# Performance work log

Hardware: AMD Instinct MI355X
Metric: run time of the kernel (lower is better)

The kernel has to match this reference:

```python
import jax, jax.numpy as jnp
import numpy as np

BLOCK = 256


def setup_inputs() -> dict:
    key = jax.random.key(0)
    ks = jax.random.split(key, 6)
    b, n, hid = 2, 4096, 2048
    h, d = 16, 128
    x = jax.random.normal(ks[0], (b, n, hid), dtype=jnp.float32)
    slope_rate = jax.random.uniform(ks[1], (h, 1, 1), dtype=jnp.float32)
    Wqkv = jax.random.normal(ks[2], (3 * h * d, hid), dtype=jnp.float32) * 0.02
    Wg = jax.random.normal(ks[3], (h * d, hid), dtype=jnp.float32) * 0.02
    norm_w = jnp.ones((h * d,), dtype=jnp.float32)
    Wo = jax.random.normal(ks[4], (hid, h * d), dtype=jnp.float32) * 0.02
    return {"x": x, "slope_rate": slope_rate, "Wqkv": Wqkv, "Wg": Wg, "norm_w": norm_w, "Wo": Wo}


def reference(x, slope_rate, Wqkv, Wg, norm_w, Wo):
    b, n, hid = x.shape
    h = slope_rate.shape[0]
    d = Wqkv.shape[0] // (3 * h)
    nb = n // BLOCK

    qkv = jax.nn.silu(x @ Wqkv.T).reshape(b, n, h, 3 * d)
    q, k, v = jnp.split(qkv, 3, axis=-1)           # each (b, n, h, d)
    # -> (b, h, n, d)
    q = q.transpose(0, 2, 1, 3)
    k = k.transpose(0, 2, 1, 3)
    v = v.transpose(0, 2, 1, 3)

    s = slope_rate.astype(jnp.float32)             # (h, 1, 1)
    arr = jnp.arange(1, BLOCK + 1, dtype=jnp.float32)
    q_decay = jnp.exp(-s * arr[:, None])           # (h, BLOCK, 1)
    k_decay = jnp.exp(-s * (BLOCK - arr[:, None])) # (h, BLOCK, 1)
    idx = arr[:, None] - arr[None, :]              # (BLOCK, BLOCK)
    diag_decay = jnp.where(idx >= 0, jnp.exp(-s * idx), 0.0)  # (h, BLOCK, BLOCK)
    block_decay = jnp.exp(-s * BLOCK)              # (h, 1, 1)

    # chunk into blocks: (nb, b, h, BLOCK, d)
    def chunk(t):
        return t.reshape(b, h, nb, BLOCK, d).transpose(2, 0, 1, 3, 4)
    qc, kc, vc = chunk(q), chunk(k), chunk(v)

    def step(kv, qkv_blk):
        qi, ki, vi = qkv_blk
        # inter-block: decayed query against running kv state
        out_nd = jnp.einsum('bhmd,bhde->bhme', qi * q_decay, kv)
        # intra-block: decay-masked quadratic attention
        qk = jnp.einsum('bhmd,bhnd->bhmn', qi, ki) * diag_decay
        out_d = jnp.einsum('bhmn,bhne->bhme', qk, vi)
        kv_new = block_decay * kv + jnp.einsum('bhmd,bhme->bhde', ki * k_decay, vi)
        return kv_new, out_nd + out_d

    kv0 = jnp.zeros((b, h, d, d), dtype=jnp.float32)
    _, out_blocks = jax.lax.scan(step, kv0, (qc, kc, vc))  # (nb, b, h, BLOCK, d)

    out = out_blocks.transpose(1, 2, 0, 3, 4).reshape(b, h, n, d)
    out = out.transpose(0, 2, 1, 3).reshape(b, n, h * d)  # b n (h d)

    # RMSNorm
    eps = jnp.finfo(jnp.float32).eps
    rms = jax.lax.rsqrt(jnp.mean(out * out, axis=-1, keepdims=True) + eps)
    out = out * rms * norm_w

    gate = jax.nn.sigmoid(x @ Wg.T)
    return (gate * out) @ Wo.T
```

## Files before the change

kernel.cpp:

```cpp
#include <hip/hip_runtime.h>
#include <stdint.h>

typedef __attribute__((ext_vector_type(8))) short short8;
typedef __attribute__((ext_vector_type(4))) float f32x4;

#define DEV static __device__ __forceinline__

DEV float b2f(unsigned short u) {
  unsigned x = ((unsigned)u) << 16;
  return __builtin_bit_cast(float, x);
}
DEV unsigned short f2b(float f) {
  unsigned x = __builtin_bit_cast(unsigned, f);
  return (unsigned short)((x + 0x7fffu + ((x >> 16) & 1u)) >> 16);
}
DEV void gload16(const unsigned short* g, unsigned short* l) {
  __builtin_amdgcn_global_load_lds((const __attribute__((address_space(1))) void*)g,
                                   (__attribute__((address_space(3))) void*)l, 16, 0, 0);
}
#define MFMA(a, b, c) __builtin_amdgcn_mfma_f32_16x16x32_bf16(a, b, c, 0, 0, 0)
#define BARRIER                          \
  asm volatile("" ::: "memory");         \
  __builtin_amdgcn_s_barrier();          \
  asm volatile("" ::: "memory")

__global__ __launch_bounds__(256) void k_f2b4(const float* __restrict__ x,
                                              const float* __restrict__ wqkv,
                                              const float* __restrict__ wg,
                                              const float* __restrict__ wo,
                                              unsigned short* __restrict__ dst) {
  long gi = ((long)blockIdx.x * 256 + threadIdx.x) * 4;
  const float* src;
  long off;
  if (gi < 16777216L) { src = x; off = gi; }
  else if (gi < 29360128L) { src = wqkv; off = gi - 16777216L; }
  else if (gi < 33554432L) { src = wg; off = gi - 29360128L; }
  else { src = wo; off = gi - 33554432L; }
  float4 f = *(const float4*)(src + off);
  ushort4 o;
  o.x = f2b(f.x); o.y = f2b(f.y); o.z = f2b(f.z); o.w = f2b(f.w);
  *(ushort4*)(dst + gi) = o;
}

template <int MODE>
__global__ __launch_bounds__(512, 2) void k_gemm(
    const unsigned short* __restrict__ A, const unsigned short* __restrict__ B0,
    const unsigned short* __restrict__ B1,
    unsigned short* __restrict__ o_q, unsigned short* __restrict__ o_k,
    unsigned short* __restrict__ o_v, unsigned short* __restrict__ o_g,
    float* __restrict__ o_f) {
  const int K = 2048, NT = 64;
  __shared__ unsigned short sm[65536];
  int tid = threadIdx.x, w = tid >> 6, lane = tid & 63;
  int wm = w >> 2, wn = w & 3;
  int l15 = lane & 15, l4 = lane >> 4;
  int xcd = blockIdx.x & 7, sub = blockIdx.x >> 3;
  int tm = xcd * 4 + (sub & 3), tn = sub >> 2;
  int brow = tm << 8, bcol = tn << 8;
  const unsigned short* Ab = A + (size_t)brow * K;
  const unsigned short* Bb = (MODE == 1 || bcol < 6144) ? (B0 + (size_t)bcol * K)
                                                        : (B1 + (size_t)(bcol - 6144) * K);
  f32x4 acc[8][4];
#pragma unroll
  for (int m = 0; m < 8; m++)
#pragma unroll
    for (int n = 0; n < 4; n++) acc[m][n] = (f32x4)0.f;

  int rdA[4], rdB[4];
  const int bslotb = (wn >> 1) ? 24576 : 8192;
  const int bposb = (wn & 1) * 64;
#pragma unroll
  for (int fi = 0; fi < 4; ++fi) {
    int posA = wm * 64 + fi * 16 + l15;
    rdA[fi] = posA * 64 + ((l4 ^ ((posA >> 1) & 3)) << 4);
    int posB = bposb + fi * 16 + l15;
    rdB[fi] = bslotb + posB * 64 + ((l4 ^ ((posB >> 1) & 3)) << 4);
  }
  const unsigned short* gP[4];
  {
    int pos = tid >> 2, pb = tid & 3;
    int scol = (pb ^ ((pos >> 1) & 3)) << 3;
#pragma unroll
    for (int s = 0; s < 4; ++s) {
      const unsigned short* gb = (s & 1) ? Bb : Ab;
      int ro = (s >> 1) << 7;
      gP[s] = gb + (size_t)(ro + pos) * K + scol;
    }
  }
  const int dLb = tid * 16;

  auto stage = [&](int bufbyte) {
#pragma unroll
    for (int s = 0; s < 4; ++s) {
      gload16(gP[s], (unsigned short*)((char*)sm + bufbyte + s * 8192 + dLb));
      gP[s] += 32;
    }
  };

  stage(0);
  stage(32768);
  asm volatile("s_waitcnt vmcnt(4)" ::: "memory");
  BARRIER;

  int b0 = 0, b1 = 32768, b2 = 65536;
  for (int T = 0; T < NT; ++T) {
    stage(b2);
    const char* smb = (const char*)sm + b0;
    short8 bfr[4], afA[4], afB[4];
#pragma unroll
    for (int nj = 0; nj < 4; ++nj) bfr[nj] = *(const short8*)(smb + rdB[nj]);
#pragma unroll
    for (int fi = 0; fi < 4; ++fi) afA[fi] = *(const short8*)(smb + rdA[fi]);
#pragma unroll
    for (int fi = 0; fi < 4; ++fi) afB[fi] = *(const short8*)(smb + (rdA[fi] + 16384));
    __builtin_amdgcn_s_setprio(1);
#pragma unroll
    for (int mi = 0; mi < 4; ++mi)
#pragma unroll
      for (int nj = 0; nj < 4; ++nj) acc[mi][nj] = MFMA(afA[mi], bfr[nj], acc[mi][nj]);
#pragma unroll
    for (int mi = 0; mi < 4; ++mi)
#pragma unroll
      for (int nj = 0; nj < 4; ++nj) acc[4 + mi][nj] = MFMA(afB[mi], bfr[nj], acc[4 + mi][nj]);
    __builtin_amdgcn_s_setprio(0);
    asm volatile("s_waitcnt vmcnt(4)" ::: "memory");
    BARRIER;
    int t = b0; b0 = b1; b1 = b2; b2 = t;
  }
  asm volatile("s_waitcnt vmcnt(0)" ::: "memory");
  BARRIER;

  if (MODE == 0) {
#pragma unroll
    for (int mf = 0; mf < 8; ++mf) {
      int rowb = (mf >> 2) * 128 + wm * 64 + (mf & 3) * 16 + l4 * 4;
#pragma unroll
      for (int ni = 0; ni < 4; ++ni) {
        int cx = wn * 64 + ((ni ^ l4) << 4) + l15;
        int colg = bcol + wn * 64 + ni * 16 + l15;
#pragma unroll
        for (int r = 0; r < 4; ++r) {
          float v = acc[mf][ni][r];
          float a = (colg < 6144) ? v / (1.f + __expf(-v))
                                  : 1.f / (1.f + __expf(-v));
          sm[(rowb + r) * 256 + cx] = f2b(a);
        }
      }
    }
    BARRIER;
    int rl0 = tid >> 5;
    int ch = (tid & 31) * 8;
    int cg = bcol + ch;
    unsigned short* qkvb = nullptr;
    size_t hbase = 0;
    int off = 0;
    const bool isq = (cg < 6144);
    if (isq) {
      int hh = cg / 384, dd = cg - hh * 384;
      int sel = dd >> 7;
      off = dd & 127;
      qkvb = (sel == 0) ? o_q : (sel == 1) ? o_k : o_v;
      hbase = (size_t)hh * 4096;
    }
#pragma unroll
    for (int it = 0; it < 16; ++it) {
      int rl = it * 16 + rl0;
      int cx = ch ^ (((rl >> 2) & 3) << 4);
      short8 v8 = *(const short8*)(sm + rl * 256 + cx);
      int row = brow + rl;
      if (isq) {
        int b = row >> 12, t = row & 4095;
        *(short8*)(qkvb + ((size_t)b * 65536 + hbase + t) * 128 + off) = v8;
      } else {
        *(short8*)(o_g + (size_t)row * 2048 + (cg - 6144)) = v8;
      }
    }
  } else {
#pragma unroll
    for (int mf = 0; mf < 8; ++mf)
#pragma unroll
      for (int r = 0; r < 4; ++r) {
        int row = brow + (mf >> 2) * 128 + wm * 64 + (mf & 3) * 16 + l4 * 4 + r;
#pragma unroll
        for (int ni = 0; ni < 4; ++ni) {
          int col = bcol + wn * 64 + ni * 16 + l15;
          o_f[(size_t)row * 2048 + col] = acc[mf][ni][r];
        }
      }
  }
}

__global__ __launch_bounds__(256) void k_kvblk(const unsigned short* __restrict__ kk,
                                               const unsigned short* __restrict__ vv,
                                               const float* __restrict__ slope,
                                               unsigned short* __restrict__ kvT) {
  int gid = blockIdx.x;
  int bh = gid >> 4, blk = gid & 15;
  float s = slope[bh & 15];
  __shared__ unsigned short kT[128][72];
  __shared__ unsigned short vT[128][72];
  int tid = threadIdx.x, w = tid >> 6, lane = tid & 63;
  int wrow = (w >> 1) * 64, wcol = (w & 1) * 64;
  f32x4 acc[4][4];
#pragma unroll
  for (int m = 0; m < 4; m++)
#pragma unroll
    for (int n = 0; n < 4; n++) acc[m][n] = (f32x4)0.f;
  const unsigned short* kb = kk + ((size_t)bh * 4096 + blk * 256) * 128;
  const unsigned short* vb = vv + ((size_t)bh * 4096 + blk * 256) * 128;
  int tt = tid & 63, c0 = (tid >> 6) * 32;
  for (int tc = 0; tc < 4; ++tc) {
    __syncthreads();
    int tg = tc * 64 + tt;
    float kd = __expf(-s * (float)(255 - tg));
#pragma unroll
    for (int g = 0; g < 4; ++g) {
      int c = c0 + g * 8;
      short8 k8 = *(const short8*)(kb + (size_t)tg * 128 + c);
      short8 v8 = *(const short8*)(vb + (size_t)tg * 128 + c);
#pragma unroll
      for (int j = 0; j < 8; ++j) {
        kT[c + j][tt] = f2b(b2f((unsigned short)k8[j]) * kd);
        vT[c + j][tt] = (unsigned short)v8[j];
      }
    }
    __syncthreads();
#pragma unroll
    for (int kx = 0; kx < 64; kx += 32) {
      int ko = kx + (lane >> 4) * 8;
      short8 af[4], bfr[4];
#pragma unroll
      for (int m = 0; m < 4; m++) af[m] = *(const short8*)&vT[wrow + m * 16 + (lane & 15)][ko];
#pragma unroll
      for (int n = 0; n < 4; n++) bfr[n] = *(const short8*)&kT[wcol + n * 16 + (lane & 15)][ko];
#pragma unroll
      for (int m = 0; m < 4; m++)
#pragma unroll
        for (int n = 0; n < 4; n++) acc[m][n] = MFMA(af[m], bfr[n], acc[m][n]);
    }
  }
  unsigned short* op = kvT + (size_t)gid * 16384;
#pragma unroll
  for (int m = 0; m < 4; m++)
#pragma unroll
    for (int r = 0; r < 4; r++) {
      int e = wrow + m * 16 + (lane >> 4) * 4 + r;
#pragma unroll
      for (int n = 0; n < 4; n++) {
        int d = wcol + n * 16 + (lane & 15);
        op[e * 128 + d] = f2b(acc[m][n][r]);
      }
    }
}

__global__ void k_scan(unsigned short* kvT, const float* __restrict__ slope) {
  int gid = blockIdx.x;
  int bh = gid >> 6;
  int eo = (gid & 63) * 256 + threadIdx.x;
  float s = slope[bh & 15];
  float bd = __expf(-s * 256.f);
  float st = 0.f;
  size_t base = (size_t)bh * 16 * 16384 + eo;
#pragma unroll
  for (int i = 0; i < 16; ++i) {
    unsigned short c = kvT[base + (size_t)i * 16384];
    kvT[base + (size_t)i * 16384] = f2b(st);
    st = bd * st + b2f(c);
  }
}

__global__ __launch_bounds__(256) void k_attn(const unsigned short* __restrict__ q,
                                              const unsigned short* __restrict__ kk,
                                              const unsigned short* __restrict__ vv,
                                              const unsigned short* __restrict__ kvT,
                                              const float* __restrict__ slope,
                                              unsigned short* __restrict__ attn) {
  int gid = blockIdx.x;
  int hf = gid & 1, blk = (gid >> 1) & 15, bh = gid >> 5;
  float s = slope[bh & 15];
  __shared__ unsigned short k_sh[64][136];
  __shared__ unsigned short vT_sh[128][72];
  __shared__ unsigned short s_sh[4][32][72];
  int tid = threadIdx.x, w = tid >> 6, lane = tid & 63;
  int mm0 = hf * 128 + w * 32;
  const unsigned short* qb = q + ((size_t)bh * 4096 + blk * 256) * 128;
  const unsigned short* kvb = kvT + (size_t)(bh * 16 + blk) * 16384;
  f32x4 acc[2][8];
#pragma unroll
  for (int m = 0; m < 2; m++)
#pragma unroll
    for (int n = 0; n < 8; n++) acc[m][n] = (f32x4)0.f;
#pragma unroll
  for (int kx = 0; kx < 128; kx += 32) {
    int ko = kx + (lane >> 4) * 8;
    short8 af[2], bfr[8];
#pragma unroll
    for (int mi = 0; mi < 2; mi++)
      af[mi] = *(const short8*)(qb + (size_t)(mm0 + mi * 16 + (lane & 15)) * 128 + ko);
#pragma unroll
    for (int ni = 0; ni < 8; ni++)
      bfr[ni] = *(const short8*)(kvb + (size_t)(ni * 16 + (lane & 15)) * 128 + ko);
#pragma unroll
    for (int mi = 0; mi < 2; mi++)
#pragma unroll
      for (int ni = 0; ni < 8; ni++) acc[mi][ni] = MFMA(af[mi], bfr[ni], acc[mi][ni]);
  }
#pragma unroll
  for (int mi = 0; mi < 2; mi++)
#pragma unroll
    for (int r = 0; r < 4; r++) {
      float qd = __expf(-s * (float)(mm0 + mi * 16 + (lane >> 4) * 4 + r + 1));
#pragma unroll
      for (int ni = 0; ni < 8; ni++) acc[mi][ni][r] *= qd;
    }
  int nchunk = 2 * (hf + 1);
  for (int tc = 0; tc < nchunk; ++tc) {
    __syncthreads();
    {
      int t2 = tid >> 2, c = (tid & 3) * 32;
      const unsigned short* kp = kk + ((size_t)bh * 4096 + blk * 256 + tc * 64 + t2) * 128 + c;
#pragma unroll
      for (int g = 0; g < 4; ++g) *(short8*)&k_sh[t2][c + g * 8] = *(const short8*)(kp + g * 8);
    }
    {
      int t2 = tid & 63, e0 = (tid >> 6) * 32;
      const unsigned short* vp = vv + ((size_t)bh * 4096 + blk * 256 + tc * 64 + t2) * 128 + e0;
#pragma unroll
      for (int g = 0; g < 4; ++g) {
        short8 v8 = *(const short8*)(vp + g * 8);
#pragma unroll
        for (int j = 0; j < 8; ++j) vT_sh[e0 + g * 8 + j][t2] = (unsigned short)v8[j];
      }
    }
    __syncthreads();
    if (tc * 64 <= mm0 + 31) {
      f32x4 sa[2][4];
#pragma unroll
      for (int m = 0; m < 2; m++)
#pragma unroll
        for (int n = 0; n < 4; n++) sa[m][n] = (f32x4)0.f;
#pragma unroll
      for (int kx = 0; kx < 128; kx += 32) {
        int ko = kx + (lane >> 4) * 8;
        short8 af[2], bfr[4];
#pragma unroll
        for (int mi = 0; mi < 2; mi++)
          af[mi] = *(const short8*)(qb + (size_t)(mm0 + mi * 16 + (lane & 15)) * 128 + ko);
#pragma unroll
        for (int ni = 0; ni < 4; ni++) bfr[ni] = *(const short8*)&k_sh[ni * 16 + (lane & 15)][ko];
#pragma unroll
        for (int mi = 0; mi < 2; mi++)
#pragma unroll
          for (int ni = 0; ni < 4; ni++) sa[mi][ni] = MFMA(af[mi], bfr[ni], sa[mi][ni]);
      }
#pragma unroll
      for (int mi = 0; mi < 2; mi++)
#pragma unroll
        for (int ni = 0; ni < 4; ni++)
#pragma unroll
          for (int r = 0; r < 4; r++) {
            int mm = mm0 + mi * 16 + (lane >> 4) * 4 + r;
            int ttg = tc * 64 + ni * 16 + (lane & 15);
            int diff = mm - ttg;
            float val = (diff >= 0) ? sa[mi][ni][r] * __expf(-s * (float)diff) : 0.f;
            s_sh[w][mi * 16 + (lane >> 4) * 4 + r][ni * 16 + (lane & 15)] = f2b(val);
          }
#pragma unroll
      for (int k2 = 0; k2 < 64; k2 += 32) {
        int ko2 = k2 + (lane >> 4) * 8;
        short8 a2[2];
#pragma unroll
        for (int mi = 0; mi < 2; mi++)
          a2[mi] = *(const short8*)&s_sh[w][mi * 16 + (lane & 15)][ko2];
#pragma unroll
        for (int ni = 0; ni < 8; ni++) {
          short8 b2 = *(const short8*)&vT_sh[ni * 16 + (lane & 15)][ko2];
#pragma unroll
          for (int mi = 0; mi < 2; mi++) acc[mi][ni] = MFMA(a2[mi], b2, acc[mi][ni]);
        }
      }
    }
  }
  int b = bh >> 4, h = bh & 15;
#pragma unroll
  for (int mi = 0; mi < 2; mi++)
#pragma unroll
    for (int r = 0; r < 4; r++) {
      int mm = mm0 + mi * 16 + (lane >> 4) * 4 + r;
      size_t rowp = ((size_t)b * 4096 + blk * 256 + mm) * 2048 + h * 128;
#pragma unroll
      for (int ni = 0; ni < 8; ni++) attn[rowp + ni * 16 + (lane & 15)] = f2b(acc[mi][ni][r]);
    }
}

__global__ __launch_bounds__(256) void k_norm(const unsigned short* __restrict__ attn,
                                              const unsigned short* __restrict__ gate,
                                              const float* __restrict__ nw,
                                              unsigned short* __restrict__ y) {
  int row = blockIdx.x;
  int tid = threadIdx.x, w = tid >> 6, lane = tid & 63;
  const unsigned short* ap = attn + (size_t)row * 2048 + tid * 8;
  const unsigned short* gp = gate + (size_t)row * 2048 + tid * 8;
  short8 a8 = *(const short8*)ap;
  float vals[8];
  float ss = 0.f;
#pragma unroll
  for (int j = 0; j < 8; ++j) {
    vals[j] = b2f((unsigned short)a8[j]);
    ss += vals[j] * vals[j];
  }
#pragma unroll
  for (int off = 32; off > 0; off >>= 1) ss += __shfl_down(ss, off, 64);
  __shared__ float red[4];
  if (lane == 0) red[w] = ss;
  __syncthreads();
  float tot = red[0] + red[1] + red[2] + red[3];
  float rms = rsqrtf(tot * (1.f / 2048.f) + 1.1920929e-07f);
  short8 g8 = *(const short8*)gp;
  short8 o;
#pragma unroll
  for (int j = 0; j < 8; ++j)
    o[j] = (short)f2b(vals[j] * rms * nw[tid * 8 + j] * b2f((unsigned short)g8[j]));
  *(short8*)(y + (size_t)row * 2048 + tid * 8) = o;
}

extern "C" void kernel_launch(void* const* d_in, const int* in_sizes, int n_in, void* d_out,
                              int out_size, void* d_ws, size_t ws_size, hipStream_t stream) {
  const float* x = (const float*)d_in[0];
  const float* slope = (const float*)d_in[1];
  const float* Wqkv = (const float*)d_in[2];
  const float* Wg = (const float*)d_in[3];
  const float* nw = (const float*)d_in[4];
  const float* Wo = (const float*)d_in[5];
  float* out = (float*)d_out;

  unsigned short* q = (unsigned short*)d_ws;
  unsigned short* k = q + 16777216;
  unsigned short* v = k + 16777216;
  unsigned short* gate = v + 16777216;
  unsigned short* xb = gate + 16777216;
  unsigned short* wqkvb = xb + 16777216;
  unsigned short* wgb = wqkvb + 12582912;
  unsigned short* wob = wgb + 4194304;
  unsigned short* kvT = wob + 4194304;
  unsigned short* attn = wqkvb;
  unsigned short* y = xb;

  k_f2b4<<<36864, 256, 0, stream>>>(x, Wqkv, Wg, Wo, xb);

  k_gemm<0><<<1024, 512, 0, stream>>>(xb, wqkvb, wgb, q, k, v, gate, nullptr);
  k_kvblk<<<512, 256, 0, stream>>>(k, v, slope, kvT);
  k_scan<<<2048, 256, 0, stream>>>(kvT, slope);
  k_attn<<<1024, 256, 0, stream>>>(q, k, v, kvT, slope, attn);
  k_norm<<<8192, 256, 0, stream>>>(attn, gate, nw, y);
  k_gemm<1><<<256, 512, 0, stream>>>(y, wob, nullptr, nullptr, nullptr, nullptr, nullptr, out);
}
```

Measured before the change: 469.9 us.

## Register-double-buffer GEMM LDS fragments; merge attention halves into 512-thread blocks

The main GEMM loop moves to a four-buffer LDS ring with three stages in flight. It is unrolled by two and ping-pongs two register fragment sets, so the LDS reads for the next tile overlap the MFMAs of the current one. The attention kernel now uses one 512-thread block per 256-row chunk instead of two 256-thread halves, so K/V tiles are loaded into LDS once and shared. Its output is staged through swizzled LDS so global stores are 16-byte coalesced rows. The cost is more LDS per block and more registers, which can lower occupancy, plus extra barriers in the attention epilogue.

After: 467.4 us. Within noise of the previous version (-0.5%).

```diff
diff --git a/kernel.cpp b/kernel.cpp
--- a/kernel.cpp
+++ b/kernel.cpp
@@ -97,38 +97,49 @@
     }
   };
 
-  stage(0);
-  stage(32768);
+  short8 cA0[4], cA1[4], cB[4], nA0[4], nA1[4], nB[4];
+#define LDTILE(dA0, dA1, dB, bufbyte)                                              \
+  {                                                                                \
+    const char* _b = (const char*)sm + (bufbyte);                                  \
+    _Pragma("unroll") for (int fi = 0; fi < 4; ++fi) {                             \
+      dB[fi] = *(const short8*)(_b + rdB[fi]);                                     \
+      dA0[fi] = *(const short8*)(_b + rdA[fi]);                                    \
+      dA1[fi] = *(const short8*)(_b + (rdA[fi] + 16384));                          \
+    }                                                                              \
+  }
+#define MFMATILE(sA0, sA1, sB)                                                     \
+  {                                                                                \
+    __builtin_amdgcn_s_setprio(1);                                                 \
+    _Pragma("unroll") for (int mi = 0; mi < 4; ++mi)                               \
+        _Pragma("unroll") for (int nj = 0; nj < 4; ++nj)                           \
+            acc[mi][nj] = MFMA(sA0[mi], sB[nj], acc[mi][nj]);                      \
+    _Pragma("unroll") for (int mi = 0; mi < 4; ++mi)                               \
+        _Pragma("unroll") for (int nj = 0; nj < 4; ++nj)                           \
+            acc[4 + mi][nj] = MFMA(sA1[mi], sB[nj], acc[4 + mi][nj]);              \
+    __builtin_amdgcn_s_setprio(0);                                                 \
+  }
+
+  stage(0); stage(32768); stage(65536);
   asm volatile("s_waitcnt vmcnt(4)" ::: "memory");
   BARRIER;
-
-  int b0 = 0, b1 = 32768, b2 = 65536;
-  for (int T = 0; T < NT; ++T) {
-    stage(b2);
-    const char* smb = (const char*)sm + b0;
-    short8 bfr[4], afA[4], afB[4];
-#pragma unroll
-    for (int nj = 0; nj < 4; ++nj) bfr[nj] = *(const short8*)(smb + rdB[nj]);
-#pragma unroll
-    for (int fi = 0; fi < 4; ++fi) afA[fi] = *(const short8*)(smb + rdA[fi]);
-#pragma unroll
-    for (int fi = 0; fi < 4; ++fi) afB[fi] = *(const short8*)(smb + (rdA[fi] + 16384));
-    __builtin_amdgcn_s_setprio(1);
-#pragma unroll
-    for (int mi = 0; mi < 4; ++mi)
-#pragma unroll
-      for (int nj = 0; nj < 4; ++nj) acc[mi][nj] = MFMA(afA[mi], bfr[nj], acc[mi][nj]);
-#pragma unroll
-    for (int mi = 0; mi < 4; ++mi)
-#pragma unroll
-      for (int nj = 0; nj < 4; ++nj) acc[4 + mi][nj] = MFMA(afB[mi], bfr[nj], acc[4 + mi][nj]);
-    __builtin_amdgcn_s_setprio(0);
+  LDTILE(cA0, cA1, cB, 0);
+
+  for (int T = 0; T < NT; T += 2) {
+    stage(((T + 3) & 3) * 32768);
+    LDTILE(nA0, nA1, nB, ((T + 1) & 3) * 32768);
+    MFMATILE(cA0, cA1, cB);
     asm volatile("s_waitcnt vmcnt(4)" ::: "memory");
     BARRIER;
-    int t = b0; b0 = b1; b1 = b2; b2 = t;
+    stage(((T + 4) & 3) * 32768);
+    LDTILE(cA0, cA1, cB, ((T + 2) & 3) * 32768);
+    MFMATILE(nA0, nA1, nB);
+    asm volatile("s_waitcnt vmcnt(4)" ::: "memory");
+    BARRIER;
   }
   asm volatile("s_waitcnt vmcnt(0)" ::: "memory");
   BARRIER;
+#undef LDTILE
+#undef MFMATILE
 
   if (MODE == 0) {
 #pragma unroll
@@ -269,20 +280,22 @@
   }
 }
 
-__global__ __launch_bounds__(256) void k_attn(const unsigned short* __restrict__ q,
+__global__ __launch_bounds__(512) void k_attn(const unsigned short* __restrict__ q,
                                               const unsigned short* __restrict__ kk,
                                               const unsigned short* __restrict__ vv,
                                               const unsigned short* __restrict__ kvT,
                                               const float* __restrict__ slope,
                                               unsigned short* __restrict__ attn) {
   int gid = blockIdx.x;
-  int hf = gid & 1, blk = (gid >> 1) & 15, bh = gid >> 5;
+  int blk = gid & 15, bh = gid >> 4;
   float s = slope[bh & 15];
-  __shared__ unsigned short k_sh[64][136];
-  __shared__ unsigned short vT_sh[128][72];
-  __shared__ unsigned short s_sh[4][32][72];
+  __shared__ char pool[72704] __attribute__((aligned(16)));
+  auto k_sh = (unsigned short(*)[136])pool;
+  auto vT_sh = (unsigned short(*)[72])(pool + 17408);
+  auto s_sh = (unsigned short(*)[32][72])(pool + 35840);
+  unsigned short* osm = (unsigned short*)pool;
   int tid = threadIdx.x, w = tid >> 6, lane = tid & 63;
-  int mm0 = hf * 128 + w * 32;
+  int mm0 = w * 32;
   const unsigned short* qb = q + ((size_t)bh * 4096 + blk * 256) * 128;
   const unsigned short* kvb = kvT + (size_t)(bh * 16 + blk) * 16384;
   f32x4 acc[2][8];
@@ -313,20 +326,19 @@
 #pragma unroll
       for (int ni = 0; ni < 8; ni++) acc[mi][ni][r] *= qd;
     }
-  int nchunk = 2 * (hf + 1);
-  for (int tc = 0; tc < nchunk; ++tc) {
+  for (int tc = 0; tc < 4; ++tc) {
     __syncthreads();
     {
-      int t2 = tid >> 2, c = (tid & 3) * 32;
+      int t2 = tid >> 3, c = (tid & 7) * 16;
       const unsigned short* kp = kk + ((size_t)bh * 4096 + blk * 256 + tc * 64 + t2) * 128 + c;
 #pragma unroll
-      for (int g = 0; g < 4; ++g) *(short8*)&k_sh[t2][c + g * 8] = *(const short8*)(kp + g * 8);
+      for (int g = 0; g < 2; ++g) *(short8*)&k_sh[t2][c + g * 8] = *(const short8*)(kp + g * 8);
     }
     {
-      int t2 = tid & 63, e0 = (tid >> 6) * 32;
+      int t2 = tid & 63, e0 = (tid >> 6) * 16;
       const unsigned short* vp = vv + ((size_t)bh * 4096 + blk * 256 + tc * 64 + t2) * 128 + e0;
 #pragma unroll
-      for (int g = 0; g < 4; ++g) {
+      for (int g = 0; g < 2; ++g) {
         short8 v8 = *(const short8*)(vp + g * 8);
 #pragma unroll
         for (int j = 0; j < 8; ++j) vT_sh[e0 + g * 8 + j][t2] = (unsigned short)v8[j];
@@ -381,16 +393,31 @@
       }
     }
   }
-  int b = bh >> 4, h = bh & 15;
+  BARRIER;
+  int l15 = lane & 15, l4 = lane >> 4;
 #pragma unroll
   for (int mi = 0; mi < 2; mi++)
 #pragma unroll
-    for (int r = 0; r < 4; r++) {
-      int mm = mm0 + mi * 16 + (lane >> 4) * 4 + r;
-      size_t rowp = ((size_t)b * 4096 + blk * 256 + mm) * 2048 + h * 128;
-#pragma unroll
-      for (int ni = 0; ni < 8; ni++) attn[rowp + ni * 16 + (lane & 15)] = f2b(acc[mi][ni][r]);
-    }
+    for (int ni = 0; ni < 8; ni++) {
+      int cx = ((ni * 16 + l15) ^ (l4 << 4));
+      int rowb = w * 32 + mi * 16 + l4 * 4;
+#pragma unroll
+      for (int r = 0; r < 4; r++) osm[(rowb + r) * 128 + cx] = f2b(acc[mi][ni][r]);
+    }
+  BARRIER;
+  {
+    int b = bh >> 4, h = bh & 15;
+    int rl0 = tid >> 4;
+    int c = tid & 15;
+#pragma unroll
+    for (int it = 0; it < 8; ++it) {
+      int rl = it * 32 + rl0;
+      int e = (c * 8) ^ (((rl >> 2) & 3) << 4);
+      short8 v8 = *(const short8*)(osm + rl * 128 + e);
+      size_t rowp = ((size_t)b * 4096 + blk * 256 + rl) * 2048 + h * 128 + c * 8;
+      *(short8*)(attn + rowp) = v8;
+    }
+  }
 }
 
 __global__ __launch_bounds__(256) void k_norm(const unsigned short* __restrict__ attn,
@@ -451,7 +478,7 @@
   k_gemm<0><<<1024, 512, 0, stream>>>(xb, wqkvb, wgb, q, k, v, gate, nullptr);
   k_kvblk<<<512, 256, 0, stream>>>(k, v, slope, kvT);
   k_scan<<<2048, 256, 0, stream>>>(kvT, slope);
-  k_attn<<<1024, 256, 0, stream>>>(q, k, v, kvT, slope, attn);
+  k_attn<<<512, 512, 0, stream>>>(q, k, v, kvT, slope, attn);
   k_norm<<<8192, 256, 0, stream>>>(attn, gate, nw, y);
   k_gemm<1><<<256, 512, 0, stream>>>(y, wob, nullptr, nullptr, nullptr, nullptr, nullptr, out);
 }
```
